# Kernel optimization log

Hardware: AMD Instinct MI355X
Metric: run time of the kernel (lower is better)

## Reference

```python
import jax, jax.numpy as jnp
import numpy as np

DIM = 128
GRID = 8
RED = 16  # LCBAM channel-attention reduction
B, L = 16, 4096


def setup_inputs() -> dict:
    key = jax.random.key(0)
    ks = jax.random.split(key, 8)
    scale = 1.0 / (np.sqrt(DIM) * np.sqrt(GRID))
    return {
        "x": jax.random.normal(ks[0], (B, L, DIM), jnp.float32),
        "n1_g": jnp.ones((DIM,), jnp.float32),
        "n1_b": jnp.zeros((DIM,), jnp.float32),
        "fk1_c": jax.random.normal(ks[1], (2, DIM, DIM, GRID), jnp.float32) * scale,
        "fk1_b": jnp.zeros((DIM,), jnp.float32),
        "n2_g": jnp.ones((DIM,), jnp.float32),
        "n2_b": jnp.zeros((DIM,), jnp.float32),
        "fk2_c": jax.random.normal(ks[2], (2, DIM, DIM, GRID), jnp.float32) * scale,
        "fk2_b": jnp.zeros((DIM,), jnp.float32),
        "w1": jax.random.normal(ks[3], (DIM // RED, DIM), jnp.float32) * 0.05,  # channel-MLP reduce
        "w2": jax.random.normal(ks[4], (DIM, DIM // RED), jnp.float32) * 0.05,  # channel-MLP expand
        "conv_w": jax.random.normal(ks[5], (1, 2, 7, 7), jnp.float32) * 0.05,   # spatial-attn 7x7 conv
    }


def _layernorm(x, g, b, eps=1e-5):
    m = jnp.mean(x, axis=-1, keepdims=True)
    v = jnp.var(x, axis=-1, keepdims=True)
    return (x - m) * jax.lax.rsqrt(v + eps) * g + b


def _fkan(x, coeffs, bias):
    # x: (B,L,I); coeffs: (2,O,I,G)
    k = jnp.arange(1, GRID + 1, dtype=x.dtype)          # (G,)
    ang = x[..., None] * k                               # (B,L,I,G)
    y = jnp.einsum("blig,oig->blo", jnp.cos(ang), coeffs[0])
    y = y + jnp.einsum("blig,oig->blo", jnp.sin(ang), coeffs[1])
    return y + bias


def reference(x, n1_g, n1_b, fk1_c, fk1_b, n2_g, n2_b, fk2_c, fk2_b, w1, w2, conv_w):
    residual = x
    out = _fkan(_layernorm(x, n1_g, n1_b), fk1_c, fk1_b)
    out = jax.nn.relu(out)
    out = _fkan(_layernorm(out, n2_g, n2_b), fk2_c, fk2_b)
    b, l, c = out.shape
    x4 = out.reshape(b, c, 1, l)  # faithful to torch .view (raw reshape, not transpose)
    # LCBAM channel attention: avg+max pool -> shared MLP -> sigmoid
    avg = jnp.mean(x4, axis=(2, 3))   # (B,C)
    mx = jnp.max(x4, axis=(2, 3))     # (B,C)
    mlp = lambda v: jax.nn.relu(v @ w1.T) @ w2.T
    ca = jax.nn.sigmoid(mlp(avg) + mlp(mx))[:, :, None, None]
    x4 = x4 * ca
    # LCBAM spatial attention: channel mean/max -> 7x7 conv -> sigmoid
    s_in = jnp.concatenate([jnp.mean(x4, axis=1, keepdims=True),
                            jnp.max(x4, axis=1, keepdims=True)], axis=1)  # (B,2,1,L)
    sa = jax.lax.conv_general_dilated(s_in, conv_w, (1, 1), ((3, 3), (3, 3)))
    x4 = x4 * jax.nn.sigmoid(sa)
    out = x4.reshape(b, l, c)
    return residual + out
```

## Files before the change

kernel.cpp:

```cpp
#include <hip/hip_runtime.h>
#include <math.h>

typedef unsigned short ushort_t;
typedef unsigned int uint_t;

#define DIMC 128
#define NB 16
#define NL 4096

using f32x4 = __attribute__((ext_vector_type(4))) float;
using bf16x8 = __attribute__((ext_vector_type(8))) short;

__device__ __forceinline__ ushort_t bf16rne(float f) {
  uint_t b = __float_as_uint(f);
  b += 0x7fffu + ((b >> 16) & 1u);
  return (ushort_t)(b >> 16);
}

__device__ __forceinline__ uint_t pkbf(float lo, float hi) {
  union { __bf16 h[2]; uint_t u; } u;
  u.h[0] = (__bf16)lo;
  u.h[1] = (__bf16)hi;
  return u.u;
}

__device__ __forceinline__ float bf2f(ushort_t u) {
  return __uint_as_float(((uint_t)u) << 16);
}

__global__ __launch_bounds__(256) void prep_coef_k(const float* __restrict__ fk1,
                                                   const float* __restrict__ fk2,
                                                   ushort_t* __restrict__ coefT) {
  int idx = blockIdx.x * 256 + threadIdx.x;
  int layer = idx >> 15;
  int rem = idx & 32767;
  int ci = rem >> 11;
  int n = (rem >> 8) & 7;
  int s = (rem >> 6) & 3;
  int l = rem & 63;
  int o = n * 16 + (l & 15);
  int kbase = ci * 128 + s * 32 + (l >> 4) * 8;
  const float* src = layer ? fk2 : fk1;
  uint_t p[4];
#pragma unroll
  for (int jj = 0; jj < 4; ++jj) {
    int k0 = kbase + jj * 2;
    int t0 = k0 & 1, g0 = (k0 >> 1) & 7, i0 = k0 >> 4;
    int k1 = k0 + 1;
    int t1 = k1 & 1, g1 = (k1 >> 1) & 7, i1 = k1 >> 4;
    ushort_t a = bf16rne(src[((t0 * DIMC + o) * DIMC + i0) * 8 + g0]);
    ushort_t b = bf16rne(src[((t1 * DIMC + o) * DIMC + i1) * 8 + g1]);
    p[jj] = (uint_t)a | ((uint_t)b << 16);
  }
  uint4 w;
  w.x = p[0]; w.y = p[1]; w.z = p[2]; w.w = p[3];
  *(uint4*)&coefT[idx * 8] = w;
}

constexpr int SX = 129;

__global__ __launch_bounds__(256, 2) void fkan_main_k(
    const float* __restrict__ x,
    const float* __restrict__ n1g, const float* __restrict__ n1b,
    const float* __restrict__ fk1b,
    const float* __restrict__ n2g, const float* __restrict__ n2b,
    const float* __restrict__ fk2b,
    const ushort_t* __restrict__ coefT,
    ushort_t* __restrict__ out2,
    float* __restrict__ chanSum, float* __restrict__ chanMax) {

  __shared__ float xln[128 * SX];
  __shared__ __align__(16) ushort_t feat[4][1024];

  const int tid = threadIdx.x;
  const int bid = blockIdx.x;
  const int lane = tid & 63;
  const int wid = tid >> 6;
  const int rowBase = wid * 32;
  const size_t tileBase = (size_t)bid * 128 * DIMC;

  {
    const float4* src = (const float4*)(x + tileBase + (size_t)rowBase * DIMC);
#pragma unroll
    for (int j = 0; j < 16; ++j) {
      int idx = j * 64 + lane;
      float4 v = src[idx];
      float* dst = &xln[(rowBase + (idx >> 5)) * SX + (idx & 31) * 4];
      dst[0] = v.x; dst[1] = v.y; dst[2] = v.z; dst[3] = v.w;
    }
  }

  auto layernorm = [&](const float* gg, const float* bb) {
    float g0 = gg[lane], g1 = gg[lane + 64];
    float be0 = bb[lane], be1 = bb[lane + 64];
#pragma unroll
    for (int j = 0; j < 32; ++j) {
      int t = rowBase + j;
      float v0 = xln[t * SX + lane], v1 = xln[t * SX + 64 + lane];
      float s = v0 + v1, q = v0 * v0 + v1 * v1;
#pragma unroll
      for (int m = 1; m < 64; m <<= 1) {
        s += __shfl_xor(s, m, 64);
        q += __shfl_xor(q, m, 64);
      }
      float mean = s * (1.0f / DIMC);
      float var = q * (1.0f / DIMC) - mean * mean;
      float rr = rsqrtf(var + 1e-5f);
      xln[t * SX + lane] = (v0 - mean) * rr * g0 + be0;
      xln[t * SX + 64 + lane] = (v1 - mean) * rr * g1 + be1;
    }
  };

  layernorm(n1g, n1b);

  auto featgen_s = [&](int cj, int s) {
    const int tl = lane & 31;
    const int ch = lane >> 5;
    float a = xln[(rowBase + tl) * SX + cj * 8 + s * 2 + ch];
    float s1, c1;
    __sincosf(a, &s1, &c1);
    uint_t p0 = pkbf(c1, s1);
    float ck = c1, sk = s1, cn, sn;
    cn = ck * c1 - sk * s1; sn = sk * c1 + ck * s1; ck = cn; sk = sn;
    uint_t p1 = pkbf(ck, sk);
    cn = ck * c1 - sk * s1; sn = sk * c1 + ck * s1; ck = cn; sk = sn;
    uint_t p2 = pkbf(ck, sk);
    cn = ck * c1 - sk * s1; sn = sk * c1 + ck * s1; ck = cn; sk = sn;
    uint_t p3 = pkbf(ck, sk);
    cn = ck * c1 - sk * s1; sn = sk * c1 + ck * s1; ck = cn; sk = sn;
    uint_t p4 = pkbf(ck, sk);
    cn = ck * c1 - sk * s1; sn = sk * c1 + ck * s1; ck = cn; sk = sn;
    uint_t p5 = pkbf(ck, sk);
    cn = ck * c1 - sk * s1; sn = sk * c1 + ck * s1; ck = cn; sk = sn;
    uint_t p6 = pkbf(ck, sk);
    cn = ck * c1 - sk * s1; sn = sk * c1 + ck * s1; ck = cn; sk = sn;
    uint_t p7 = pkbf(ck, sk);
    int mm = tl >> 4;
    int slot = (tl & 15) + (ch << 5);
    ushort_t* base = &feat[wid][mm * 512];
    uint4 w0; w0.x = p0; w0.y = p1; w0.z = p2; w0.w = p3;
    uint4 w1; w1.x = p4; w1.y = p5; w1.z = p6; w1.w = p7;
    *(uint4*)&base[slot * 8] = w0;
    *(uint4*)&base[(slot + 16) * 8] = w1;
  };

  f32x4 acc[8][2];

  auto ldB = [&](const ushort_t* cbase, int ci, int s, bf16x8 (&bf)[8]) {
#pragma unroll
    for (int nn = 0; nn < 8; ++nn)
      bf[nn] = *(const bf16x8*)(cbase +
          (size_t)((((ci * 8 + nn) * 4 + s) << 6) + lane) * 8);
  };

  auto mfma16 = [&](bf16x8 (&bf)[8]) {
    bf16x8 af0 = *(const bf16x8*)&feat[wid][lane * 8];
    bf16x8 af1 = *(const bf16x8*)&feat[wid][512 + lane * 8];
    __builtin_amdgcn_s_setprio(1);
#pragma unroll
    for (int nn = 0; nn < 8; ++nn) {
      acc[nn][0] = __builtin_amdgcn_mfma_f32_16x16x32_bf16(af0, bf[nn],
                                                           acc[nn][0], 0, 0, 0);
      acc[nn][1] = __builtin_amdgcn_mfma_f32_16x16x32_bf16(af1, bf[nn],
                                                           acc[nn][1], 0, 0, 0);
    }
    __builtin_amdgcn_s_setprio(0);
  };

  auto run_layer = [&](const ushort_t* cbase) {
#pragma unroll
    for (int nn = 0; nn < 8; ++nn)
#pragma unroll
      for (int mm = 0; mm < 2; ++mm) acc[nn][mm] = (f32x4)(0.f);
    bf16x8 bfE[8], bfO[8];
    ldB(cbase, 0, 0, bfE);
#pragma unroll 1
    for (int ci = 0; ci < 16; ++ci) {
      featgen_s(ci, 0); ldB(cbase, ci, 1, bfO); mfma16(bfE);
      featgen_s(ci, 1); ldB(cbase, ci, 2, bfE); mfma16(bfO);
      featgen_s(ci, 2); ldB(cbase, ci, 3, bfO); mfma16(bfE);
      featgen_s(ci, 3); ldB(cbase, ci + 1, 0, bfE); mfma16(bfO);
    }
  };

  run_layer(coefT);

#pragma unroll
  for (int nn = 0; nn < 8; ++nn) {
    int o = nn * 16 + (lane & 15);
    float bia = fk1b[o];
#pragma unroll
    for (int mm = 0; mm < 2; ++mm) {
      int trow = rowBase + mm * 16 + (lane >> 4) * 4;
#pragma unroll
      for (int r = 0; r < 4; ++r)
        xln[(trow + r) * SX + o] = fmaxf(acc[nn][mm][r] + bia, 0.f);
    }
  }

  layernorm(n2g, n2b);

  run_layer(coefT + 262144);

  float ls = 0.f, lm = -INFINITY;
#pragma unroll
  for (int nn = 0; nn < 8; ++nn) {
    int o = nn * 16 + (lane & 15);
    float bia = fk2b[o];
#pragma unroll
    for (int mm = 0; mm < 2; ++mm) {
      int trow = rowBase + mm * 16 + (lane >> 4) * 4;
#pragma unroll
      for (int r = 0; r < 4; ++r) {
        float v = acc[nn][mm][r] + bia;
        out2[tileBase + (size_t)(trow + r) * DIMC + o] = bf16rne(v);
        ls += v;
        lm = fmaxf(lm, v);
      }
    }
  }
#pragma unroll
  for (int m = 1; m < 64; m <<= 1) {
    ls += __shfl_xor(ls, m, 64);
    lm = fmaxf(lm, __shfl_xor(lm, m, 64));
  }
  if (lane == 0) {
    chanSum[bid * 4 + wid] = ls;
    chanMax[bid * 4 + wid] = lm;
  }
}

__global__ __launch_bounds__(128) void tail_k(
    const float* __restrict__ x, const ushort_t* __restrict__ out2,
    const float* __restrict__ chanSum, const float* __restrict__ chanMax,
    const float* __restrict__ w1, const float* __restrict__ w2,
    const float* __restrict__ convw, float* __restrict__ dout) {
  int b = blockIdx.x >> 5;
  int t = blockIdx.x & 31;
  int c = threadIdx.x;
  __shared__ float avs[DIMC], mxs[DIMC], hh[16], cas[DIMC];
  __shared__ float sM[134], sX[134];

  avs[c] = chanSum[b * DIMC + c] * (1.0f / NL);
  mxs[c] = chanMax[b * DIMC + c];
  __syncthreads();
  if (c < 16) {
    const float* v = (c < 8) ? avs : mxs;
    float a = 0.f;
    for (int i = 0; i < DIMC; ++i) a += v[i] * w1[(c & 7) * DIMC + i];
    hh[c] = fmaxf(a, 0.f);
  }
  __syncthreads();
  {
    float z = 0.f;
#pragma unroll
    for (int r = 0; r < 8; ++r) z += (hh[r] + hh[8 + r]) * w2[c * 8 + r];
    cas[c] = 1.0f / (1.0f + expf(-z));
  }
  __syncthreads();

  const ushort_t* o2b = out2 + (size_t)b * NL * DIMC;
  float s = 0.f, m = -INFINITY;
#pragma unroll 4
  for (int c4 = 0; c4 < 128; ++c4) {
    float v = bf2f(o2b[(size_t)(c4 * 32 + t) * DIMC + c]) * cas[c4];
    s += v;
    m = fmaxf(m, v);
  }
  sM[c + 3] = s * (1.0f / DIMC);
  sX[c + 3] = m;
  if (c < 6) {
    bool left = c < 3;
    int tp = left ? t - 1 : t + 1;
    int cc = left ? 125 + c : c - 3;
    int di = left ? c : 131 + (c - 3);
    float ss = 0.f, mm2 = -INFINITY;
    if (tp >= 0 && tp < 32) {
#pragma unroll 4
      for (int c4 = 0; c4 < 128; ++c4) {
        float v = bf2f(o2b[(size_t)(c4 * 32 + tp) * DIMC + cc]) * cas[c4];
        ss += v;
        mm2 = fmaxf(mm2, v);
      }
      sM[di] = ss * (1.0f / DIMC);
      sX[di] = mm2;
    } else {
      sM[di] = 0.f;
      sX[di] = 0.f;
    }
  }
  __syncthreads();

  float sa = 0.f;
#pragma unroll
  for (int d = 0; d < 7; ++d)
    sa += convw[21 + d] * sM[c + d] + convw[70 + d] * sX[c + d];
  float sig = 1.0f / (1.0f + expf(-sa));

  const float* xb = x + (size_t)b * NL * DIMC;
  float* db = dout + (size_t)b * NL * DIMC;
#pragma unroll 2
  for (int c4 = 0; c4 < 128; ++c4) {
    size_t idx = (size_t)(c4 * 32 + t) * DIMC + c;
    db[idx] = xb[idx] + bf2f(o2b[idx]) * cas[c4] * sig;
  }
}

extern "C" void kernel_launch(void* const* d_in, const int* in_sizes, int n_in,
                              void* d_out, int out_size, void* d_ws, size_t ws_size,
                              hipStream_t stream) {
  const float* x = (const float*)d_in[0];
  const float* n1g = (const float*)d_in[1];
  const float* n1b = (const float*)d_in[2];
  const float* fk1c = (const float*)d_in[3];
  const float* fk1b = (const float*)d_in[4];
  const float* n2g = (const float*)d_in[5];
  const float* n2b = (const float*)d_in[6];
  const float* fk2c = (const float*)d_in[7];
  const float* fk2b = (const float*)d_in[8];
  const float* w1 = (const float*)d_in[9];
  const float* w2 = (const float*)d_in[10];
  const float* convw = (const float*)d_in[11];

  ushort_t* out2 = (ushort_t*)d_ws;
  ushort_t* coefT = out2 + 8388608;
  float* chanSum = (float*)(coefT + 524288);
  float* chanMax = chanSum + 2048;
  float* dout = (float*)d_out;

  prep_coef_k<<<256, 256, 0, stream>>>(fk1c, fk2c, coefT);
  fkan_main_k<<<512, 256, 0, stream>>>(x, n1g, n1b, fk1b, n2g, n2b,
                                       fk2b, coefT, out2, chanSum, chanMax);
  tail_k<<<NB * 32, 128, 0, stream>>>(x, out2, chanSum, chanMax, w1, w2, convw, dout);
}
```

Measured before the change: 154.2 us.

## Generate MFMA A-fragments in registers instead of staging features through LDS

The Fourier feature generator now produces each lane's bf16x8 A-operand fragment directly in registers, matching the MFMA 16x16x32 layout, so the per-wave LDS feature buffer and its write/read round trip are gone. The A fragments for the next k-step are produced alongside the B loads, giving a software pipeline in which feature generation overlaps the current MFMAs. The cost is twice the sincos/rotation work per lane, because each lane computes all eight harmonics but keeps only half. It also adds register pressure from the extra live fragments, which may hurt occupancy under launch_bounds(256,2).

After: 185.9 us. 20.6% more time.

```diff
diff --git a/kernel.cpp b/kernel.cpp
--- a/kernel.cpp
+++ b/kernel.cpp
@@ -70,7 +70,6 @@
     float* __restrict__ chanSum, float* __restrict__ chanMax) {
 
   __shared__ float xln[128 * SX];
-  __shared__ __align__(16) ushort_t feat[4][1024];
 
   const int tid = threadIdx.x;
   const int bid = blockIdx.x;
@@ -113,10 +112,12 @@
 
   layernorm(n1g, n1b);
 
-  auto featgen_s = [&](int cj, int s) {
-    const int tl = lane & 31;
-    const int ch = lane >> 5;
-    float a = xln[(rowBase + tl) * SX + cj * 8 + s * 2 + ch];
+  const int hi = lane >> 4;
+  const int hb = hi & 1;
+  const float* xfr = &xln[(rowBase + (lane & 15)) * SX + (hi >> 1)];
+
+  auto featfrag = [&](int ci, int s, int mm) -> bf16x8 {
+    float a = xfr[mm * 16 * SX + ci * 8 + s * 2];
     float s1, c1;
     __sincosf(a, &s1, &c1);
     uint_t p0 = pkbf(c1, s1);
@@ -135,13 +136,12 @@
     uint_t p6 = pkbf(ck, sk);
     cn = ck * c1 - sk * s1; sn = sk * c1 + ck * s1; ck = cn; sk = sn;
     uint_t p7 = pkbf(ck, sk);
-    int mm = tl >> 4;
-    int slot = (tl & 15) + (ch << 5);
-    ushort_t* base = &feat[wid][mm * 512];
-    uint4 w0; w0.x = p0; w0.y = p1; w0.z = p2; w0.w = p3;
-    uint4 w1; w1.x = p4; w1.y = p5; w1.z = p6; w1.w = p7;
-    *(uint4*)&base[slot * 8] = w0;
-    *(uint4*)&base[(slot + 16) * 8] = w1;
+    union { uint_t u[4]; bf16x8 v; } r;
+    r.u[0] = hb ? p4 : p0;
+    r.u[1] = hb ? p5 : p1;
+    r.u[2] = hb ? p6 : p2;
+    r.u[3] = hb ? p7 : p3;
+    return r.v;
   };
 
   f32x4 acc[8][2];
@@ -153,15 +153,13 @@
           (size_t)((((ci * 8 + nn) * 4 + s) << 6) + lane) * 8);
   };
 
-  auto mfma16 = [&](bf16x8 (&bf)[8]) {
-    bf16x8 af0 = *(const bf16x8*)&feat[wid][lane * 8];
-    bf16x8 af1 = *(const bf16x8*)&feat[wid][512 + lane * 8];
+  auto mfma16 = [&](bf16x8 a0, bf16x8 a1, bf16x8 (&bf)[8]) {
     __builtin_amdgcn_s_setprio(1);
 #pragma unroll
     for (int nn = 0; nn < 8; ++nn) {
-      acc[nn][0] = __builtin_amdgcn_mfma_f32_16x16x32_bf16(af0, bf[nn],
+      acc[nn][0] = __builtin_amdgcn_mfma_f32_16x16x32_bf16(a0, bf[nn],
                                                            acc[nn][0], 0, 0, 0);
-      acc[nn][1] = __builtin_amdgcn_mfma_f32_16x16x32_bf16(af1, bf[nn],
+      acc[nn][1] = __builtin_amdgcn_mfma_f32_16x16x32_bf16(a1, bf[nn],
                                                            acc[nn][1], 0, 0, 0);
     }
     __builtin_amdgcn_s_setprio(0);
@@ -173,13 +171,32 @@
 #pragma unroll
       for (int mm = 0; mm < 2; ++mm) acc[nn][mm] = (f32x4)(0.f);
     bf16x8 bfE[8], bfO[8];
+    bf16x8 aE0, aE1, aO0, aO1;
     ldB(cbase, 0, 0, bfE);
+    aE0 = featfrag(0, 0, 0);
+    aE1 = featfrag(0, 0, 1);
 #pragma unroll 1
     for (int ci = 0; ci < 16; ++ci) {
-      featgen_s(ci, 0); ldB(cbase, ci, 1, bfO); mfma16(bfE);
-      featgen_s(ci, 1); ldB(cbase, ci, 2, bfE); mfma16(bfO);
-      featgen_s(ci, 2); ldB(cbase, ci, 3, bfO); mfma16(bfE);
-      featgen_s(ci, 3); ldB(cbase, ci + 1, 0, bfE); mfma16(bfO);
+      ldB(cbase, ci, 1, bfO);
+      aO0 = featfrag(ci, 1, 0);
+      aO1 = featfrag(ci, 1, 1);
+      mfma16(aE0, aE1, bfE);
+
+      ldB(cbase, ci, 2, bfE);
+      aE0 = featfrag(ci, 2, 0);
+      aE1 = featfrag(ci, 2, 1);
+      mfma16(aO0, aO1, bfO);
+
+      ldB(cbase, ci, 3, bfO);
+      aO0 = featfrag(ci, 3, 0);
+      aO1 = featfrag(ci, 3, 1);
+      mfma16(aE0, aE1, bfE);
+
+      int cn2 = (ci + 1) & 15;
+      ldB(cbase, cn2, 0, bfE);
+      aE0 = featfrag(cn2, 0, 0);
+      aE1 = featfrag(cn2, 0, 1);
+      mfma16(aO0, aO1, bfO);
     }
   };
 
```
